# Kernel tuning notes

Hardware: AMD Instinct MI355X
Metric: run time of the kernel (lower is better)

Reference implementation:

```python
import jax, jax.numpy as jnp
import numpy as np

H = 187          # BATTLEFIELD_HEXES
MS = 20          # MAX_STACKS
MOB = 10         # MAX_OBSTACLES
D = 128          # d_model
NH = 4           # n_heads
NL = 4           # n_layers
CE = 16          # creature_embed_dim
NAT = 5          # NUM_ACTION_TYPES
NCT = 256        # NUM_CREATURE_TYPES
HEXC = 29        # HEX_CONTINUOUS_DIM
B = 1024


def _ln(x, g, b):
    m = x.mean(-1, keepdims=True)
    v = jnp.mean((x - m) ** 2, -1, keepdims=True)
    return (x - m) / jnp.sqrt(v + 1e-5) * g + b


def _mlp(x, w1, b1, w2, b2):
    return jax.nn.relu(x @ w1.T + b1) @ w2.T + b2


def _forward(p, n_stacks):
    scalars = p['scalars']
    s = p['stacks']
    pos = s[:, :, 18].astype(jnp.int32)                       # POSITION
    alive = s[:, :, 23]                                       # ALIVE
    idx_mask = jnp.arange(MS)[None, :] < n_stacks             # (B, MS)
    valid = (pos >= 0) & (pos < H) & (alive >= 0.5) & idx_mask
    max_hp = jnp.maximum(s[:, :, 4], 1.0)
    is_active = (s[:, :, 0] == scalars[:, 2:3]).astype(jnp.float32)
    is_ally = (s[:, :, 20] == scalars[:, 3:4]).astype(jnp.float32)
    zeros = jnp.zeros_like(alive)
    feat = jnp.stack([
        jnp.ones_like(alive), s[:, :, 2] / 1000.0, s[:, :, 3] / max_hp,
        s[:, :, 8] / 100.0, s[:, :, 9] / 100.0, s[:, :, 10] / 100.0, s[:, :, 11] / 100.0,
        s[:, :, 12] / 100.0, s[:, :, 13] / 100.0, s[:, :, 14] / 100.0, s[:, :, 15] / 100.0,
        s[:, :, 16] / 20.0, s[:, :, 17] / 20.0, s[:, :, 20], is_ally, alive,
        s[:, :, 24], s[:, :, 25], s[:, :, 26], s[:, :, 27], s[:, :, 28], s[:, :, 29],
        s[:, :, 30], s[:, :, 31] / 30.0, s[:, :, 33] / 5.0, s[:, :, 34] / 10.0,
        is_active, zeros, zeros], axis=-1)                    # (B, MS, 29)
    bidx = jnp.arange(B)[:, None]
    safe_pos = jnp.where(valid, pos, H)                       # dummy slot H for invalid
    hex_cont = jnp.zeros((B, H + 1, HEXC)).at[bidx, safe_pos].set(
        jnp.where(valid[..., None], feat, 0.0))[:, :H]
    cid = jnp.minimum(s[:, :, 1].astype(jnp.int32), NCT - 1)
    cids = jnp.zeros((B, H + 1), jnp.int32).at[bidx, safe_pos].set(
        jnp.where(valid, cid, 0))[:, :H]
    hex_cont = hex_cont.at[:, :, 27].set(p['reachable_hexes'])
    opos = p['obstacles'][:, :, 2].astype(jnp.int32)
    ovalid = (p['obstacles'][:, :, 0] > 0) & (opos >= 0) & (opos < H)
    obs_ch = jnp.zeros((B, H + 1)).at[bidx, jnp.where(ovalid, opos, H)].max(
        ovalid.astype(jnp.float32))[:, :H]
    hex_cont = hex_cont.at[:, :, 28].set(obs_ch)
    hex_feat = jnp.concatenate([hex_cont, p['creature_emb'][cids]], -1)   # (B,H,45)

    hex_tok = _ln(hex_feat @ p['hex_proj_w'].T + p['hex_proj_b'],
                  p['hex_ln_g'], p['hex_ln_b'])
    hex_tok = hex_tok + p['hex_pos_emb'][None] + p['tok_type_emb'][0]

    sc = scalars
    atk = jnp.stack([sc[:, 8], sc[:, 11] / 300.0, sc[:, 10] / 10.0, sc[:, 12] / 10.0,
                     jnp.zeros(B)], -1)
    dfn = jnp.stack([sc[:, 14], sc[:, 17] / 300.0, sc[:, 16] / 10.0, sc[:, 18] / 10.0,
                     jnp.ones(B)], -1)
    atk_t = _ln(atk @ p['hero_proj_w'].T + p['hero_proj_b'], p['hero_ln_g'], p['hero_ln_b']) + p['tok_type_emb'][1]
    def_t = _ln(dfn @ p['hero_proj_w'].T + p['hero_proj_b'], p['hero_ln_g'], p['hero_ln_b']) + p['tok_type_emb'][2]
    tokens = jnp.concatenate([hex_tok, atk_t[:, None], def_t[:, None]], 1)  # (B,189,D)

    gfeat = jnp.stack([sc[:, 1] / 50.0, sc[:, 4] / 10.0, sc[:, 5] / 10.0, sc[:, 6], sc[:, 3]], -1)
    tokens = tokens + (gfeat @ p['global_w'].T + p['global_b'])[:, None]

    S = tokens.shape[1]
    hd = D // NH
    for l in range(NL):  # pre-LN transformer encoder (eval mode, no dropout)
        x = _ln(tokens, p['tf_ln1_g'][l], p['tf_ln1_b'][l])
        qkv = x @ p['tf_qkv_w'][l].T + p['tf_qkv_b'][l]
        q, k, v = jnp.split(qkv, 3, -1)
        rs = lambda t: t.reshape(B, S, NH, hd).transpose(0, 2, 1, 3)
        q, k, v = rs(q), rs(k), rs(v)
        att = jax.nn.softmax(jnp.einsum('bhqd,bhkd->bhqk', q, k) / jnp.sqrt(float(hd)), -1)
        o = jnp.einsum('bhqk,bhkd->bhqd', att, v).transpose(0, 2, 1, 3).reshape(B, S, D)
        tokens = tokens + o @ p['tf_o_w'][l].T + p['tf_o_b'][l]
        y = _ln(tokens, p['tf_ln2_g'][l], p['tf_ln2_b'][l])
        tokens = tokens + jax.nn.relu(y @ p['tf_ff1_w'][l].T + p['tf_ff1_b'][l]) @ p['tf_ff2_w'][l].T + p['tf_ff2_b'][l]
    tokens = _ln(tokens, p['post_ln_g'], p['post_ln_b'])

    hex_out = tokens[:, :H]
    pooled = tokens.mean(1)
    action_type_logits = _mlp(pooled, p['at_w1'], p['at_b1'], p['at_w2'], p['at_b2'])
    hex_logits = _mlp(hex_out, p['hex_w1'], p['hex_b1'], p['hex_w2'], p['hex_b2']).squeeze(-1)
    tgt_tok = jnp.take_along_axis(hex_out, jnp.clip(pos, 0, H - 1)[..., None], axis=1)  # (B,MS,D)
    tgt = _mlp(tgt_tok, p['tg_w1'], p['tg_b1'], p['tg_w2'], p['tg_b2']).squeeze(-1)
    target_logits = jnp.where(valid, tgt, -1e9)
    value = _mlp(pooled, p['val_w1'], p['val_b1'], p['val_w2'], p['val_b2']).squeeze(-1)
    return (action_type_logits, hex_logits, target_logits, value)


def setup_inputs() -> dict:
    key = jax.random.key(0)
    ks = iter(jax.random.split(key, 64))
    nk = lambda: next(ks)
    _p = lambda shape: 0.02 * jax.random.normal(nk(), shape, dtype=jnp.float32)

    scalars = jax.random.uniform(nk(), (B, 19)) * 10.0
    scalars = scalars.at[:, 2].set(jax.random.randint(nk(), (B,), 0, MS).astype(jnp.float32))
    scalars = scalars.at[:, 3].set(jax.random.randint(nk(), (B,), 0, 2).astype(jnp.float32))

    stacks = jax.random.uniform(nk(), (B, MS, 35)) * 50.0
    perm = jax.vmap(lambda k: jax.random.permutation(k, H)[:MS])(jax.random.split(nk(), B))
    stacks = stacks.at[:, :, 18].set(perm.astype(jnp.float32))          # unique positions
    stacks = stacks.at[:, :, 23].set((jax.random.uniform(nk(), (B, MS)) > 0.2).astype(jnp.float32))
    stacks = stacks.at[:, :, 1].set(jax.random.randint(nk(), (B, MS), 0, NCT).astype(jnp.float32))
    stacks = stacks.at[:, :, 0].set(jnp.broadcast_to(jnp.arange(MS, dtype=jnp.float32), (B, MS)))
    stacks = stacks.at[:, :, 20].set(jax.random.randint(nk(), (B, MS), 0, 2).astype(jnp.float32))

    obstacles = jnp.stack([
        jax.random.randint(nk(), (B, MOB), 0, 3).astype(jnp.float32),
        jnp.zeros((B, MOB)),
        jax.random.randint(nk(), (B, MOB), 0, H).astype(jnp.float32)], -1)
    reachable_hexes = (jax.random.uniform(nk(), (B, H)) > 0.5).astype(jnp.float32)
    n_stacks = jax.random.randint(nk(), (B, 1), 1, MS + 1)

    inp = dict(scalars=scalars, stacks=stacks, obstacles=obstacles,
               reachable_hexes=reachable_hexes, n_stacks=n_stacks)
    inp['creature_emb'] = _p((NCT, CE)).at[0].set(0.0)   # padding_idx=0
    inp['hex_pos_emb'] = _p((H, D))
    inp['tok_type_emb'] = _p((3, D))
    inp['hex_proj_w'] = _p((D, HEXC + CE)); inp['hex_proj_b'] = _p((D,))
    inp['hex_ln_g'] = jnp.ones(D); inp['hex_ln_b'] = jnp.zeros(D)
    inp['hero_proj_w'] = _p((D, 5)); inp['hero_proj_b'] = _p((D,))
    inp['hero_ln_g'] = jnp.ones(D); inp['hero_ln_b'] = jnp.zeros(D)
    inp['global_w'] = _p((D, 5)); inp['global_b'] = _p((D,))
    inp['tf_ln1_g'] = jnp.ones((NL, D)); inp['tf_ln1_b'] = jnp.zeros((NL, D))
    inp['tf_qkv_w'] = _p((NL, 3 * D, D)); inp['tf_qkv_b'] = _p((NL, 3 * D))
    inp['tf_o_w'] = _p((NL, D, D)); inp['tf_o_b'] = _p((NL, D))
    inp['tf_ln2_g'] = jnp.ones((NL, D)); inp['tf_ln2_b'] = jnp.zeros((NL, D))
    inp['tf_ff1_w'] = _p((NL, 4 * D, D)); inp['tf_ff1_b'] = _p((NL, 4 * D))
    inp['tf_ff2_w'] = _p((NL, D, 4 * D)); inp['tf_ff2_b'] = _p((NL, D))
    inp['post_ln_g'] = jnp.ones(D); inp['post_ln_b'] = jnp.zeros(D)
    inp['at_w1'] = _p((D, D)); inp['at_b1'] = _p((D,)); inp['at_w2'] = _p((NAT, D)); inp['at_b2'] = _p((NAT,))
    inp['hex_w1'] = _p((D // 2, D)); inp['hex_b1'] = _p((D // 2,)); inp['hex_w2'] = _p((1, D // 2)); inp['hex_b2'] = _p((1,))
    inp['tg_w1'] = _p((D // 2, D)); inp['tg_b1'] = _p((D // 2,)); inp['tg_w2'] = _p((1, D // 2)); inp['tg_b2'] = _p((1,))
    inp['val_w1'] = _p((D, D)); inp['val_b1'] = _p((D,)); inp['val_w2'] = _p((1, D)); inp['val_b2'] = _p((1,))
    return inp


def reference(scalars, stacks, obstacles, reachable_hexes, n_stacks, creature_emb, hex_pos_emb, tok_type_emb, hex_proj_w, hex_proj_b, hex_ln_g, hex_ln_b, hero_proj_w, hero_proj_b, hero_ln_g, hero_ln_b, global_w, global_b, tf_ln1_g, tf_ln1_b, tf_qkv_w, tf_qkv_b, tf_o_w, tf_o_b, tf_ln2_g, tf_ln2_b, tf_ff1_w, tf_ff1_b, tf_ff2_w, tf_ff2_b, post_ln_g, post_ln_b, at_w1, at_b1, at_w2, at_b2, hex_w1, hex_b1, hex_w2, hex_b2, tg_w1, tg_b1, tg_w2, tg_b2, val_w1, val_b1, val_w2, val_b2):
    fl = dict(locals())
    ns = fl.pop('n_stacks')
    return _forward(fl, ns)
```

## Files before the change

kernel.cpp:

```cpp
#include <hip/hip_runtime.h>
#include <hip/hip_bf16.h>

#define DEV static __device__ __forceinline__

typedef __attribute__((ext_vector_type(8))) short bf16x8;
typedef __attribute__((ext_vector_type(4))) float f32x4;
#define MFMA16 __builtin_amdgcn_mfma_f32_16x16x32_bf16

DEV unsigned short f2bf_rn(float x) {
  unsigned u = __float_as_uint(x);
  u = u + 0x7fffu + ((u >> 16) & 1u);
  return (unsigned short)(u >> 16);
}
DEV unsigned pack2(float a, float b) {
  return (unsigned)f2bf_rn(a) | ((unsigned)f2bf_rn(b) << 16);
}
DEV float lo2f(unsigned w) { return __uint_as_float(w << 16); }
DEV float hi2f(unsigned w) { return __uint_as_float(w & 0xffff0000u); }

constexpr int H_ = 187, MS_ = 20, MOB_ = 10, D_ = 128, NH_ = 4, NL_ = 4,
              CE_ = 16, NAT_ = 5, NCT_ = 256, HEXC_ = 29, B_ = 1024;
constexpr int S_ = H_ + 2;
constexpr int ST = 68;
constexpr int PST = 36;
constexpr int VTS = 100;

constexpr int VT_OFF   = 192 * PST;
constexpr int CORR_OFF = VT_OFF + 32 * VTS;
constexpr int LSUM_OFF = CORR_OFF + 192;
constexpr int GV_OFF   = LSUM_OFF + 192;
constexpr int PO_OFF   = GV_OFF + 128;
constexpr int H1_OFF   = PO_OFF + 128;
constexpr int H2_OFF   = H1_OFF + 128;

constexpr int OFF_HEX = B_ * NAT_;
constexpr int OFF_TGT = OFF_HEX + B_ * H_;
constexpr int OFF_VAL = OFF_TGT + B_ * MS_;

constexpr float SCALE = 0.17677669529663687f;

constexpr int WS_Q = 0;
constexpr int WS_O = WS_Q + 4 * 384 * 128;
constexpr int WS_F1 = WS_O + 4 * 128 * 128;
constexpr int WS_F2 = WS_F1 + 4 * 512 * 128;
constexpr int WS_TOT = WS_F2 + 4 * 128 * 512;

struct Params {
  const float *scalars, *stacks, *obstacles, *reach;
  const int  *n_stacks;
  const float *cemb, *pos_emb, *tte;
  const float *hexW, *hexB, *hexG, *hexBe;
  const float *heroW, *heroB, *heroG, *heroBe;
  const float *gW, *gB;
  const float *ln1g, *ln1b, *qkvW, *qkvB, *oW, *oB;
  const float *ln2g, *ln2b, *f1W, *f1B, *f2W, *f2B;
  const float *plng, *plnb;
  const float *atW1, *atB1, *atW2, *atB2;
  const float *hxW1, *hxB1, *hxW2, *hxB2;
  const float *tgW1, *tgB1, *tgW2, *tgB2;
  const float *vlW1, *vlB1, *vlW2, *vlB2;
  const unsigned short *wsb;
  float *out;
};

DEV bf16x8 ldAx(const unsigned* buf, int stride, int mbase, int cbase, int lane) {
  return *(const bf16x8*)(buf + (mbase + (lane & 15)) * stride + cbase +
                          ((lane >> 4) << 2));
}
DEV bf16x8 ldBw(const float* q) {
  bf16x8 r;
#pragma unroll
  for (int j = 0; j < 8; ++j) r[j] = (short)f2bf_rn(q[j]);
  return r;
}
template <bool WSB>
DEV bf16x8 ldB(const unsigned short* wb, const float* wf, int off) {
  if constexpr (WSB) return *(const bf16x8*)(wb + off);
  else return ldBw(wf + off);
}

__global__ __launch_bounds__(256) void convw_kernel(const float *qkv,
                                                    const float *o,
                                                    const float *f1,
                                                    const float *f2,
                                                    unsigned short *ws) {
  int i = blockIdx.x * 256 + threadIdx.x;
  if (i < WS_O) ws[i] = f2bf_rn(qkv[i - WS_Q]);
  else if (i < WS_F1) ws[i] = f2bf_rn(o[i - WS_O]);
  else if (i < WS_F2) ws[i] = f2bf_rn(f1[i - WS_F1]);
  else if (i < WS_TOT) ws[i] = f2bf_rn(f2[i - WS_F2]);
}

template <bool WSB>
__global__ __launch_bounds__(768, 1) void battle_kernel(Params p) {
  __shared__ __align__(16) unsigned tokp[192 * ST];
  __shared__ __align__(16) unsigned xln[192 * ST];
  __shared__ __align__(16) unsigned area[192 * ST];
  __shared__ int svalid[MS_], sposc[MS_];

  const int b = blockIdx.x;
  const int tid = threadIdx.x;
  const int lane = tid & 63;
  const int wave = tid >> 6;
  const bool hasrow = tid < S_;
  const float *sc = p.scalars + b * 19;

  float *areaF = (float *)area;
  unsigned short *tok16 = (unsigned short *)tokp;
  unsigned short *xln16 = (unsigned short *)xln;
  unsigned short *P16 = (unsigned short *)area;
  unsigned short *vt16 = (unsigned short *)(area + VT_OFF);

  float *hexcont = (float *)area;
  int   *cids    = (int *)area + 5440;
  float *obsch   = (float *)area + 5632;

  if (tid < D_) {
    float g0 = sc[1] * 0.02f, g1 = sc[4] * 0.1f, g2 = sc[5] * 0.1f;
    float g3 = sc[6], g4 = sc[3];
    const float *w = p.gW + tid * 5;
    areaF[GV_OFF + tid] = p.gB[tid] + g0 * w[0] + g1 * w[1] + g2 * w[2] +
                          g3 * w[3] + g4 * w[4];
  }
  for (int i = tid; i < H_ * HEXC_; i += 768) hexcont[i] = 0.f;
  for (int i = tid; i < H_; i += 768) { cids[i] = 0; obsch[i] = 0.f; }
  if (tid >= 189 && tid < 192) {
    for (int c = 0; c < 64; ++c) tokp[tid * ST + c] = 0u;
  }
  __syncthreads();

  if (tid < MS_) {
    const float *st = p.stacks + (b * MS_ + tid) * 35;
    int pos = (int)st[18];
    float alive = st[23];
    int ns = p.n_stacks[b];
    bool valid = (pos >= 0) && (pos < H_) && (alive >= 0.5f) && (tid < ns);
    svalid[tid] = valid ? 1 : 0;
    sposc[tid] = min(max(pos, 0), H_ - 1);
    if (valid) {
      float maxhp = fmaxf(st[4], 1.0f);
      float *hc = hexcont + pos * HEXC_;
      hc[0] = 1.0f;
      hc[1] = st[2] * 1e-3f;
      hc[2] = st[3] / maxhp;
      hc[3] = st[8] * 0.01f;  hc[4] = st[9] * 0.01f;
      hc[5] = st[10] * 0.01f; hc[6] = st[11] * 0.01f;
      hc[7] = st[12] * 0.01f; hc[8] = st[13] * 0.01f;
      hc[9] = st[14] * 0.01f; hc[10] = st[15] * 0.01f;
      hc[11] = st[16] * 0.05f; hc[12] = st[17] * 0.05f;
      float s20 = st[20];
      hc[13] = s20;
      hc[14] = (s20 == sc[3]) ? 1.f : 0.f;
      hc[15] = alive;
      hc[16] = st[24]; hc[17] = st[25]; hc[18] = st[26];
      hc[19] = st[27]; hc[20] = st[28]; hc[21] = st[29];
      hc[22] = st[30];
      hc[23] = st[31] * (1.f / 30.f);
      hc[24] = st[33] * 0.2f;
      hc[25] = st[34] * 0.1f;
      hc[26] = (st[0] == sc[2]) ? 1.f : 0.f;
      hc[27] = 0.f; hc[28] = 0.f;
      cids[pos] = min((int)st[1], NCT_ - 1);
    }
  }
  if (tid >= 64 && tid < 64 + MOB_) {
    const float *ob = p.obstacles + (b * MOB_ + (tid - 64)) * 3;
    int opos = (int)ob[2];
    if (ob[0] > 0.f && opos >= 0 && opos < H_) obsch[opos] = 1.0f;
  }
  __syncthreads();

  if (tid < H_) {
    const int r = tid;
    float f[HEXC_ + CE_];
#pragma unroll
    for (int c = 0; c < HEXC_; ++c) f[c] = hexcont[r * HEXC_ + c];
    f[27] = p.reach[b * H_ + r];
    f[28] = obsch[r];
    int cid = cids[r];
#pragma unroll
    for (int e = 0; e < CE_; ++e) f[HEXC_ + e] = p.cemb[cid * CE_ + e];
    float sum = 0.f;
    for (int d2 = 0; d2 < 64; ++d2) {
      const float *w0 = p.hexW + (2 * d2) * 45;
      const float *w1 = w0 + 45;
      float a0 = p.hexB[2 * d2], a1 = 0.f, a2 = 0.f, a3 = 0.f;
      float b0 = p.hexB[2 * d2 + 1], b1 = 0.f, b2 = 0.f, b3 = 0.f;
#pragma unroll
      for (int k = 0; k < 44; k += 4) {
        a0 = fmaf(f[k], w0[k], a0);       a1 = fmaf(f[k + 1], w0[k + 1], a1);
        a2 = fmaf(f[k + 2], w0[k + 2], a2); a3 = fmaf(f[k + 3], w0[k + 3], a3);
        b0 = fmaf(f[k], w1[k], b0);       b1 = fmaf(f[k + 1], w1[k + 1], b1);
        b2 = fmaf(f[k + 2], w1[k + 2], b2); b3 = fmaf(f[k + 3], w1[k + 3], b3);
      }
      a0 = fmaf(f[44], w0[44], a0);
      b0 = fmaf(f[44], w1[44], b0);
      float va = (a0 + a1) + (a2 + a3), vb = (b0 + b1) + (b2 + b3);
      tokp[r * ST + d2] = pack2(va, vb);
      sum += va + vb;
    }
    float m = sum * (1.f / 128.f);
    float var = 0.f;
#pragma unroll 4
    for (int d2 = 0; d2 < 64; ++d2) {
      unsigned w = tokp[r * ST + d2];
      float t0 = lo2f(w) - m, t1 = hi2f(w) - m;
      var = fmaf(t0, t0, var); var = fmaf(t1, t1, var);
    }
    float rs = rsqrtf(var * (1.f / 128.f) + 1e-5f);
#pragma unroll 2
    for (int d2 = 0; d2 < 64; ++d2) {
      unsigned w = tokp[r * ST + d2];
      int d = 2 * d2;
      float v0 = (lo2f(w) - m) * rs * p.hexG[d] + p.hexBe[d] +
                 p.pos_emb[r * D_ + d] + p.tte[d] + areaF[GV_OFF + d];
      float v1 = (hi2f(w) - m) * rs * p.hexG[d + 1] + p.hexBe[d + 1] +
                 p.pos_emb[r * D_ + d + 1] + p.tte[d + 1] + areaF[GV_OFF + d + 1];
      tokp[r * ST + d2] = pack2(v0, v1);
    }
  } else if (tid < S_) {
    const int which = tid - H_;
    float f0, f1, f2, f3, f4;
    if (which == 0) {
      f0 = sc[8];  f1 = sc[11] * (1.f / 300.f);
      f2 = sc[10] * 0.1f; f3 = sc[12] * 0.1f; f4 = 0.f;
    } else {
      f0 = sc[14]; f1 = sc[17] * (1.f / 300.f);
      f2 = sc[16] * 0.1f; f3 = sc[18] * 0.1f; f4 = 1.f;
    }
    const int r = tid;
    float sum = 0.f;
    for (int d2 = 0; d2 < 64; ++d2) {
      const float *w0 = p.heroW + (2 * d2) * 5;
      const float *w1 = w0 + 5;
      float va = p.heroB[2 * d2] + f0 * w0[0] + f1 * w0[1] + f2 * w0[2] + f3 * w0[3] + f4 * w0[4];
      float vb = p.heroB[2 * d2 + 1] + f0 * w1[0] + f1 * w1[1] + f2 * w1[2] + f3 * w1[3] + f4 * w1[4];
      tokp[r * ST + d2] = pack2(va, vb);
      sum += va + vb;
    }
    float m = sum * (1.f / 128.f);
    float var = 0.f;
    for (int d2 = 0; d2 < 64; ++d2) {
      unsigned w = tokp[r * ST + d2];
      float t0 = lo2f(w) - m, t1 = hi2f(w) - m;
      var = fmaf(t0, t0, var); var = fmaf(t1, t1, var);
    }
    float rs = rsqrtf(var * (1.f / 128.f) + 1e-5f);
    for (int d2 = 0; d2 < 64; ++d2) {
      unsigned w = tokp[r * ST + d2];
      int d = 2 * d2;
      float v0 = (lo2f(w) - m) * rs * p.heroG[d] + p.heroBe[d] +
                 p.tte[(1 + which) * D_ + d] + areaF[GV_OFF + d];
      float v1 = (hi2f(w) - m) * rs * p.heroG[d + 1] + p.heroBe[d + 1] +
                 p.tte[(1 + which) * D_ + d + 1] + areaF[GV_OFF + d + 1];
      tokp[r * ST + d2] = pack2(v0, v1);
    }
  }

  const int lrow = tid >> 2;
  const int lsub = tid & 3;

  for (int l = 0; l < NL_; ++l) {
    const float *ln1g = p.ln1g + l * D_, *ln1b = p.ln1b + l * D_;
    const float *qkvW = p.qkvW + l * 3 * D_ * D_, *qkvB = p.qkvB + l * 3 * D_;
    const float *oW = p.oW + l * D_ * D_, *oB = p.oB + l * D_;
    const float *ln2g = p.ln2g + l * D_, *ln2b = p.ln2b + l * D_;
    const float *f1W = p.f1W + l * 4 * D_ * D_, *f1B = p.f1B + l * 4 * D_;
    const float *f2W = p.f2W + l * 4 * D_ * D_, *f2B = p.f2B + l * D_;
    const unsigned short *qkvWb = p.wsb + WS_Q + l * 384 * 128;
    const unsigned short *oWb = p.wsb + WS_O + l * 128 * 128;
    const unsigned short *f1Wb = p.wsb + WS_F1 + l * 512 * 128;
    const unsigned short *f2Wb = p.wsb + WS_F2 + l * 128 * 512;

    __syncthreads();

    if (lrow < S_) {
      float s = 0.f;
#pragma unroll
      for (int i = 0; i < 16; ++i) {
        unsigned w = tokp[lrow * ST + lsub * 16 + i];
        s += lo2f(w) + hi2f(w);
      }
      s += __shfl_xor(s, 1); s += __shfl_xor(s, 2);
      float m = s * (1.f / 128.f);
      float v = 0.f;
#pragma unroll
      for (int i = 0; i < 16; ++i) {
        unsigned w = tokp[lrow * ST + lsub * 16 + i];
        float t0 = lo2f(w) - m, t1 = hi2f(w) - m;
        v = fmaf(t0, t0, v); v = fmaf(t1, t1, v);
      }
      v += __shfl_xor(v, 1); v += __shfl_xor(v, 2);
      float rs = rsqrtf(v * (1.f / 128.f) + 1e-5f);
#pragma unroll
      for (int i = 0; i < 16; ++i) {
        int d2 = lsub * 16 + i, d = 2 * d2;
        unsigned w = tokp[lrow * ST + d2];
        xln[lrow * ST + d2] = pack2((lo2f(w) - m) * rs * ln1g[d] + ln1b[d],
                                    (hi2f(w) - m) * rs * ln1g[d + 1] + ln1b[d + 1]);
      }
    } else {
#pragma unroll
      for (int i = 0; i < 16; ++i) xln[lrow * ST + lsub * 16 + i] = 0u;
    }
    __syncthreads();

    f32x4 oacc[4][2];

#pragma unroll
    for (int h = 0; h < NH_; ++h) {
#pragma unroll
      for (int nd = 0; nd < 2; ++nd) oacc[h][nd] = {0.f, 0.f, 0.f, 0.f};

      {
        int ntg = wave >> 1, mh = wave & 1;
        int nrow0, c16 = 0, isV = 0, ntd = 0;
        if (ntg < 2)      { nrow0 = h * 32 + ntg * 16;            c16 = ntg * 16; }
        else if (ntg < 4) { nrow0 = 128 + h * 32 + (ntg - 2) * 16; c16 = 32 + (ntg - 2) * 16; }
        else              { nrow0 = 256 + h * 32 + (ntg - 4) * 16; isV = 1; ntd = ntg - 4; }
        int roff = (nrow0 + (lane & 15)) * 128;
        int koff = (lane >> 4) << 3;
        bf16x8 b0 = ldB<WSB>(qkvWb, qkvW, roff + koff);
        bf16x8 b1 = ldB<WSB>(qkvWb, qkvW, roff + 32 + koff);
        bf16x8 b2 = ldB<WSB>(qkvWb, qkvW, roff + 64 + koff);
        bf16x8 b3 = ldB<WSB>(qkvWb, qkvW, roff + 96 + koff);
        float bv = qkvB[nrow0 + (lane & 15)];
        int col16 = c16 + (lane & 15);
#pragma unroll 1
        for (int mt = mh * 6; mt < mh * 6 + 6; ++mt) {
          f32x4 acc = {bv, bv, bv, bv};
          acc = MFMA16(ldAx(xln, ST, mt * 16, 0, lane), b0, acc, 0, 0, 0);
          acc = MFMA16(ldAx(xln, ST, mt * 16, 16, lane), b1, acc, 0, 0, 0);
          acc = MFMA16(ldAx(xln, ST, mt * 16, 32, lane), b2, acc, 0, 0, 0);
          acc = MFMA16(ldAx(xln, ST, mt * 16, 48, lane), b3, acc, 0, 0, 0);
          int rb = mt * 16 + ((lane >> 4) << 2);
          if (!isV) {
#pragma unroll
            for (int g = 0; g < 4; ++g)
              P16[(rb + g) * (PST * 2) + col16] = f2bf_rn(acc[g]);
          } else {
#pragma unroll
            for (int g = 0; g < 4; ++g)
              vt16[(ntd * 16 + (lane & 15)) * (VTS * 2) + rb + g] = f2bf_rn(acc[g]);
          }
        }
      }
      __syncthreads();

      bf16x8 qf = ldAx(area, PST, wave * 16, 0, lane);
      bf16x8 kf[12];
#pragma unroll
      for (int nt = 0; nt < 12; ++nt)
        kf[nt] = ldAx(area, PST, nt * 16, 16, lane);
      float mrun = -1e30f, lrun = 0.f;
      const int srow = wave * 16 + (lane & 15);
      const int ssub = lane >> 4;
      __syncthreads();

#pragma unroll
      for (int t = 0; t < 3; ++t) {
        {
          int rb = wave * 16 + ((lane >> 4) << 2);
#pragma unroll
          for (int ntl = 0; ntl < 4; ++ntl) {
            f32x4 s = {0.f, 0.f, 0.f, 0.f};
            s = MFMA16(qf, kf[t * 4 + ntl], s, 0, 0, 0);
            int col16 = ntl * 16 + (lane & 15);
#pragma unroll
            for (int g = 0; g < 4; ++g)
              P16[(rb + g) * (PST * 2) + col16] = f2bf_rn(s[g]);
          }
        }
        {
          float tm = -1e30f;
          int cb = ssub * 8;
#pragma unroll
          for (int i = 0; i < 8; ++i) {
            int c2 = cb + i;
            unsigned w = area[srow * PST + c2];
            float v0 = lo2f(w) * SCALE, v1 = hi2f(w) * SCALE;
            if (t == 2 && c2 == 30) v1 = -1e30f;
            if (t == 2 && c2 == 31) { v0 = -1e30f; v1 = -1e30f; }
            tm = fmaxf(tm, fmaxf(v0, v1));
          }
          tm = fmaxf(tm, __shfl_xor(tm, 16));
          tm = fmaxf(tm, __shfl_xor(tm, 32));
          float mnew = fmaxf(mrun, tm);
          float corrv = __expf(mrun - mnew);
          float ts = 0.f;
#pragma unroll
          for (int i = 0; i < 8; ++i) {
            int c2 = cb + i;
            unsigned w = area[srow * PST + c2];
            float e0 = __expf(lo2f(w) * SCALE - mnew);
            float e1 = __expf(hi2f(w) * SCALE - mnew);
            if (t == 2 && c2 == 30) e1 = 0.f;
            if (t == 2 && c2 == 31) { e0 = 0.f; e1 = 0.f; }
            ts += e0 + e1;
            area[srow * PST + c2] = pack2(e0, e1);
          }
          ts += __shfl_xor(ts, 16);
          ts += __shfl_xor(ts, 32);
          lrun = lrun * corrv + ts;
          mrun = mnew;
          if (ssub == 0) {
            areaF[CORR_OFF + srow] = corrv;
            if (t == 2) areaF[LSUM_OFF + srow] = lrun;
          }
        }
        {
          int rb = wave * 16 + ((lane >> 4) << 2);
          float c0 = areaF[CORR_OFF + rb], c1 = areaF[CORR_OFF + rb + 1];
          float c2v = areaF[CORR_OFF + rb + 2], c3 = areaF[CORR_OFF + rb + 3];
#pragma unroll
          for (int nd = 0; nd < 2; ++nd) {
            f32x4 a = oacc[h][nd];
            a[0] *= c0; a[1] *= c1; a[2] *= c2v; a[3] *= c3;
#pragma unroll
            for (int kt = 0; kt < 2; ++kt) {
              bf16x8 af = ldAx(area, PST, wave * 16, kt * 16, lane);
              bf16x8 bv = *(const bf16x8*)(area + VT_OFF +
                            (nd * 16 + (lane & 15)) * VTS + t * 32 + kt * 16 +
                            ((lane >> 4) << 2));
              a = MFMA16(af, bv, a, 0, 0, 0);
            }
            oacc[h][nd] = a;
          }
          if (t == 2) {
            float i0 = 1.f / areaF[LSUM_OFF + rb];
            float i1 = 1.f / areaF[LSUM_OFF + rb + 1];
            float i2 = 1.f / areaF[LSUM_OFF + rb + 2];
            float i3 = 1.f / areaF[LSUM_OFF + rb + 3];
#pragma unroll
            for (int nd = 0; nd < 2; ++nd) {
              f32x4 a = oacc[h][nd];
              a[0] *= i0; a[1] *= i1; a[2] *= i2; a[3] *= i3;
              oacc[h][nd] = a;
            }
          }
        }
      }
      __syncthreads();
    }

#pragma unroll
    for (int h = 0; h < NH_; ++h) {
      int rb = wave * 16 + ((lane >> 4) << 2);
#pragma unroll
      for (int nd = 0; nd < 2; ++nd) {
        int col16 = h * 32 + nd * 16 + (lane & 15);
        f32x4 a = oacc[h][nd];
#pragma unroll
        for (int g = 0; g < 4; ++g)
          xln16[(rb + g) * (ST * 2) + col16] = f2bf_rn(a[g]);
      }
    }
    __syncthreads();

#pragma unroll 1
    for (int job = wave; job < 16; job += 12) {
      int nt = job >> 1, mh = job & 1;
      int roff = (nt * 16 + (lane & 15)) * 128;
      int koff = (lane >> 4) << 3;
      bf16x8 b0 = ldB<WSB>(oWb, oW, roff + koff);
      bf16x8 b1 = ldB<WSB>(oWb, oW, roff + 32 + koff);
      bf16x8 b2 = ldB<WSB>(oWb, oW, roff + 64 + koff);
      bf16x8 b3 = ldB<WSB>(oWb, oW, roff + 96 + koff);
      float bv = oB[nt * 16 + (lane & 15)];
      int col16 = nt * 16 + (lane & 15);
#pragma unroll 1
      for (int mt = mh * 6; mt < mh * 6 + 6; ++mt) {
        f32x4 acc = {bv, bv, bv, bv};
        acc = MFMA16(ldAx(xln, ST, mt * 16, 0, lane), b0, acc, 0, 0, 0);
        acc = MFMA16(ldAx(xln, ST, mt * 16, 16, lane), b1, acc, 0, 0, 0);
        acc = MFMA16(ldAx(xln, ST, mt * 16, 32, lane), b2, acc, 0, 0, 0);
        acc = MFMA16(ldAx(xln, ST, mt * 16, 48, lane), b3, acc, 0, 0, 0);
        int rb = mt * 16 + ((lane >> 4) << 2);
#pragma unroll
        for (int g = 0; g < 4; ++g) {
          int a16 = (rb + g) * (ST * 2) + col16;
          float old = __uint_as_float((unsigned)tok16[a16] << 16);
          tok16[a16] = f2bf_rn(old + acc[g]);
        }
      }
    }
    __syncthreads();

    if (lrow < S_) {
      float s = 0.f;
#pragma unroll
      for (int i = 0; i < 16; ++i) {
        unsigned w = tokp[lrow * ST + lsub * 16 + i];
        s += lo2f(w) + hi2f(w);
      }
      s += __shfl_xor(s, 1); s += __shfl_xor(s, 2);
      float m = s * (1.f / 128.f);
      float v = 0.f;
#pragma unroll
      for (int i = 0; i < 16; ++i) {
        unsigned w = tokp[lrow * ST + lsub * 16 + i];
        float t0 = lo2f(w) - m, t1 = hi2f(w) - m;
        v = fmaf(t0, t0, v); v = fmaf(t1, t1, v);
      }
      v += __shfl_xor(v, 1); v += __shfl_xor(v, 2);
      float rs = rsqrtf(v * (1.f / 128.f) + 1e-5f);
#pragma unroll
      for (int i = 0; i < 16; ++i) {
        int d2 = lsub * 16 + i, d = 2 * d2;
        unsigned w = tokp[lrow * ST + d2];
        xln[lrow * ST + d2] = pack2((lo2f(w) - m) * rs * ln2g[d] + ln2b[d],
                                    (hi2f(w) - m) * rs * ln2g[d + 1] + ln2b[d + 1]);
      }
    } else {
#pragma unroll
      for (int i = 0; i < 16; ++i) xln[lrow * ST + lsub * 16 + i] = 0u;
    }
    __syncthreads();

    const int ja = wave;
    const bool hasb = wave < 4;
    const int jb = wave + 12;
    const int nta = ja >> 1, mha = ja & 1;
    const int ntb = jb >> 1, mhb = jb & 1;
    f32x4 acca[6], accb[6];
    {
      float bva = f2B[nta * 16 + (lane & 15)];
#pragma unroll
      for (int i = 0; i < 6; ++i) acca[i] = {bva, bva, bva, bva};
      float bvb = hasb ? f2B[ntb * 16 + (lane & 15)] : 0.f;
#pragma unroll
      for (int i = 0; i < 6; ++i) accb[i] = {bvb, bvb, bvb, bvb};
    }
    for (int chunk = 0; chunk < 4; ++chunk) {
#pragma unroll 1
      for (int job = wave; job < 16; job += 12) {
        int nt = job >> 1, mh = job & 1;
        int roff = (chunk * 128 + nt * 16 + (lane & 15)) * 128;
        int koff = (lane >> 4) << 3;
        bf16x8 b0 = ldB<WSB>(f1Wb, f1W, roff + koff);
        bf16x8 b1 = ldB<WSB>(f1Wb, f1W, roff + 32 + koff);
        bf16x8 b2 = ldB<WSB>(f1Wb, f1W, roff + 64 + koff);
        bf16x8 b3 = ldB<WSB>(f1Wb, f1W, roff + 96 + koff);
        float bv = f1B[chunk * 128 + nt * 16 + (lane & 15)];
        int col16 = nt * 16 + (lane & 15);
#pragma unroll 1
        for (int mt = mh * 6; mt < mh * 6 + 6; ++mt) {
          f32x4 acc = {bv, bv, bv, bv};
          acc = MFMA16(ldAx(xln, ST, mt * 16, 0, lane), b0, acc, 0, 0, 0);
          acc = MFMA16(ldAx(xln, ST, mt * 16, 16, lane), b1, acc, 0, 0, 0);
          acc = MFMA16(ldAx(xln, ST, mt * 16, 32, lane), b2, acc, 0, 0, 0);
          acc = MFMA16(ldAx(xln, ST, mt * 16, 48, lane), b3, acc, 0, 0, 0);
          int rb = mt * 16 + ((lane >> 4) << 2);
#pragma unroll
          for (int g = 0; g < 4; ++g)
            P16[(rb + g) * (ST * 2) + col16] = f2bf_rn(fmaxf(acc[g], 0.f));
        }
      }
      __syncthreads();
      {
        int roff = (nta * 16 + (lane & 15)) * 512 + chunk * 128;
        int koff = (lane >> 4) << 3;
        bf16x8 b0 = ldB<WSB>(f2Wb, f2W, roff + koff);
        bf16x8 b1 = ldB<WSB>(f2Wb, f2W, roff + 32 + koff);
        bf16x8 b2 = ldB<WSB>(f2Wb, f2W, roff + 64 + koff);
        bf16x8 b3 = ldB<WSB>(f2Wb, f2W, roff + 96 + koff);
#pragma unroll
        for (int i = 0; i < 6; ++i) {
          int mt = mha * 6 + i;
          f32x4 a = acca[i];
          a = MFMA16(ldAx(area, ST, mt * 16, 0, lane), b0, a, 0, 0, 0);
          a = MFMA16(ldAx(area, ST, mt * 16, 16, lane), b1, a, 0, 0, 0);
          a = MFMA16(ldAx(area, ST, mt * 16, 32, lane), b2, a, 0, 0, 0);
          a = MFMA16(ldAx(area, ST, mt * 16, 48, lane), b3, a, 0, 0, 0);
          acca[i] = a;
        }
      }
      if (hasb) {
        int roff = (ntb * 16 + (lane & 15)) * 512 + chunk * 128;
        int koff = (lane >> 4) << 3;
        bf16x8 b0 = ldB<WSB>(f2Wb, f2W, roff + koff);
        bf16x8 b1 = ldB<WSB>(f2Wb, f2W, roff + 32 + koff);
        bf16x8 b2 = ldB<WSB>(f2Wb, f2W, roff + 64 + koff);
        bf16x8 b3 = ldB<WSB>(f2Wb, f2W, roff + 96 + koff);
#pragma unroll
        for (int i = 0; i < 6; ++i) {
          int mt = mhb * 6 + i;
          f32x4 a = accb[i];
          a = MFMA16(ldAx(area, ST, mt * 16, 0, lane), b0, a, 0, 0, 0);
          a = MFMA16(ldAx(area, ST, mt * 16, 16, lane), b1, a, 0, 0, 0);
          a = MFMA16(ldAx(area, ST, mt * 16, 32, lane), b2, a, 0, 0, 0);
          a = MFMA16(ldAx(area, ST, mt * 16, 48, lane), b3, a, 0, 0, 0);
          accb[i] = a;
        }
      }
      __syncthreads();
    }
    {
      int col16 = nta * 16 + (lane & 15);
#pragma unroll
      for (int i = 0; i < 6; ++i) {
        int rb = (mha * 6 + i) * 16 + ((lane >> 4) << 2);
        f32x4 a = acca[i];
#pragma unroll
        for (int g = 0; g < 4; ++g) {
          int a16 = (rb + g) * (ST * 2) + col16;
          float old = __uint_as_float((unsigned)tok16[a16] << 16);
          tok16[a16] = f2bf_rn(old + a[g]);
        }
      }
    }
    if (hasb) {
      int col16 = ntb * 16 + (lane & 15);
#pragma unroll
      for (int i = 0; i < 6; ++i) {
        int rb = (mhb * 6 + i) * 16 + ((lane >> 4) << 2);
        f32x4 a = accb[i];
#pragma unroll
        for (int g = 0; g < 4; ++g) {
          int a16 = (rb + g) * (ST * 2) + col16;
          float old = __uint_as_float((unsigned)tok16[a16] << 16);
          tok16[a16] = f2bf_rn(old + a[g]);
        }
      }
    }
  }
  __syncthreads();

  if (lrow < S_) {
    float s = 0.f;
#pragma unroll
    for (int i = 0; i < 16; ++i) {
      unsigned w = tokp[lrow * ST + lsub * 16 + i];
      s += lo2f(w) + hi2f(w);
    }
    s += __shfl_xor(s, 1); s += __shfl_xor(s, 2);
    float m = s * (1.f / 128.f);
    float v = 0.f;
#pragma unroll
    for (int i = 0; i < 16; ++i) {
      unsigned w = tokp[lrow * ST + lsub * 16 + i];
      float t0 = lo2f(w) - m, t1 = hi2f(w) - m;
      v = fmaf(t0, t0, v); v = fmaf(t1, t1, v);
    }
    v += __shfl_xor(v, 1); v += __shfl_xor(v, 2);
    float rs = rsqrtf(v * (1.f / 128.f) + 1e-5f);
#pragma unroll
    for (int i = 0; i < 16; ++i) {
      int d2 = lsub * 16 + i, d = 2 * d2;
      unsigned w = tokp[lrow * ST + d2];
      tokp[lrow * ST + d2] = pack2((lo2f(w) - m) * rs * p.plng[d] + p.plnb[d],
                                   (hi2f(w) - m) * rs * p.plng[d + 1] + p.plnb[d + 1]);
    }
  }
  __syncthreads();

  if (tid < D_) {
    const int d2 = tid >> 1;
    const bool hi = tid & 1;
    float s0 = 0.f, s1 = 0.f;
    int r = 0;
    for (; r + 2 <= S_; r += 2) {
      unsigned w0 = tokp[r * ST + d2], w1 = tokp[(r + 1) * ST + d2];
      s0 += hi ? hi2f(w0) : lo2f(w0);
      s1 += hi ? hi2f(w1) : lo2f(w1);
    }
    unsigned wl = tokp[(S_ - 1) * ST + d2];
    s0 += hi ? hi2f(wl) : lo2f(wl);
    areaF[PO_OFF + tid] = (s0 + s1) * (1.f / (float)S_);
  }
  __syncthreads();
  if (tid < D_) {
    const float *wa = p.atW1 + tid * D_;
    const float *wv = p.vlW1 + tid * D_;
    float a0 = p.atB1[tid], a1 = 0.f, vv0 = p.vlB1[tid], vv1 = 0.f;
#pragma unroll 4
    for (int k = 0; k < D_; k += 2) {
      float pk0 = areaF[PO_OFF + k], pk1 = areaF[PO_OFF + k + 1];
      a0 = fmaf(pk0, wa[k], a0);   a1 = fmaf(pk1, wa[k + 1], a1);
      vv0 = fmaf(pk0, wv[k], vv0); vv1 = fmaf(pk1, wv[k + 1], vv1);
    }
    areaF[H1_OFF + tid] = fmaxf(a0 + a1, 0.f);
    areaF[H2_OFF + tid] = fmaxf(vv0 + vv1, 0.f);
  }
  __syncthreads();

  if (tid < H_) {
    float hh[64];
#pragma unroll
    for (int j = 0; j < 64; ++j) hh[j] = p.hxB1[j];
    for (int kb = 0; kb < 8; ++kb) {
      float xr[16];
#pragma unroll
      for (int i2 = 0; i2 < 8; ++i2) {
        unsigned w = tokp[tid * ST + kb * 8 + i2];
        xr[2 * i2] = lo2f(w); xr[2 * i2 + 1] = hi2f(w);
      }
      const float *w = p.hxW1 + kb * 16;
#pragma unroll
      for (int j = 0; j < 64; ++j) {
#pragma unroll
        for (int i = 0; i < 16; ++i)
          hh[j] = fmaf(xr[i], w[j * D_ + i], hh[j]);
      }
    }
    float o = p.hxB2[0];
#pragma unroll
    for (int j = 0; j < 64; ++j) o = fmaf(fmaxf(hh[j], 0.f), p.hxW2[j], o);
    p.out[OFF_HEX + b * H_ + tid] = o;
  }
  if (tid < NAT_) {
    const float *w = p.atW2 + tid * D_;
    float o0 = p.atB2[tid], o1 = 0.f, o2 = 0.f, o3 = 0.f;
#pragma unroll 4
    for (int k = 0; k < D_; k += 4) {
      o0 = fmaf(areaF[H1_OFF + k], w[k], o0);
      o1 = fmaf(areaF[H1_OFF + k + 1], w[k + 1], o1);
      o2 = fmaf(areaF[H1_OFF + k + 2], w[k + 2], o2);
      o3 = fmaf(areaF[H1_OFF + k + 3], w[k + 3], o3);
    }
    p.out[b * NAT_ + tid] = (o0 + o1) + (o2 + o3);
  }
  if (tid == 190) {
    float o0 = p.vlB2[0], o1 = 0.f, o2 = 0.f, o3 = 0.f;
#pragma unroll 4
    for (int k = 0; k < D_; k += 4) {
      o0 = fmaf(areaF[H2_OFF + k], p.vlW2[k], o0);
      o1 = fmaf(areaF[H2_OFF + k + 1], p.vlW2[k + 1], o1);
      o2 = fmaf(areaF[H2_OFF + k + 2], p.vlW2[k + 2], o2);
      o3 = fmaf(areaF[H2_OFF + k + 3], p.vlW2[k + 3], o3);
    }
    p.out[OFF_VAL + b] = (o0 + o1) + (o2 + o3);
  }
  if (tid >= 32 && tid < 32 + MS_) {
    int si = tid - 32;
    float o;
    if (svalid[si]) {
      int r = sposc[si];
      float hh[64];
#pragma unroll
      for (int j = 0; j < 64; ++j) hh[j] = p.tgB1[j];
      for (int kb = 0; kb < 8; ++kb) {
        float xr[16];
#pragma unroll
        for (int i2 = 0; i2 < 8; ++i2) {
          unsigned w = tokp[r * ST + kb * 8 + i2];
          xr[2 * i2] = lo2f(w); xr[2 * i2 + 1] = hi2f(w);
        }
        const float *w = p.tgW1 + kb * 16;
#pragma unroll
        for (int j = 0; j < 64; ++j) {
#pragma unroll
          for (int i = 0; i < 16; ++i)
            hh[j] = fmaf(xr[i], w[j * D_ + i], hh[j]);
        }
      }
      o = p.tgB2[0];
#pragma unroll
      for (int j = 0; j < 64; ++j) o = fmaf(fmaxf(hh[j], 0.f), p.tgW2[j], o);
    } else {
      o = -1e9f;
    }
    p.out[OFF_TGT + b * MS_ + si] = o;
  }
}

extern "C" void kernel_launch(void* const* d_in, const int* in_sizes, int n_in,
                              void* d_out, int out_size, void* d_ws, size_t ws_size,
                              hipStream_t stream) {
  (void)in_sizes; (void)n_in; (void)out_size;
  Params p;
  p.scalars = (const float *)d_in[0];
  p.stacks = (const float *)d_in[1];
  p.obstacles = (const float *)d_in[2];
  p.reach = (const float *)d_in[3];
  p.n_stacks = (const int *)d_in[4];
  p.cemb = (const float *)d_in[5];
  p.pos_emb = (const float *)d_in[6];
  p.tte = (const float *)d_in[7];
  p.hexW = (const float *)d_in[8];  p.hexB = (const float *)d_in[9];
  p.hexG = (const float *)d_in[10]; p.hexBe = (const float *)d_in[11];
  p.heroW = (const float *)d_in[12]; p.heroB = (const float *)d_in[13];
  p.heroG = (const float *)d_in[14]; p.heroBe = (const float *)d_in[15];
  p.gW = (const float *)d_in[16]; p.gB = (const float *)d_in[17];
  p.ln1g = (const float *)d_in[18]; p.ln1b = (const float *)d_in[19];
  p.qkvW = (const float *)d_in[20]; p.qkvB = (const float *)d_in[21];
  p.oW = (const float *)d_in[22]; p.oB = (const float *)d_in[23];
  p.ln2g = (const float *)d_in[24]; p.ln2b = (const float *)d_in[25];
  p.f1W = (const float *)d_in[26]; p.f1B = (const float *)d_in[27];
  p.f2W = (const float *)d_in[28]; p.f2B = (const float *)d_in[29];
  p.plng = (const float *)d_in[30]; p.plnb = (const float *)d_in[31];
  p.atW1 = (const float *)d_in[32]; p.atB1 = (const float *)d_in[33];
  p.atW2 = (const float *)d_in[34]; p.atB2 = (const float *)d_in[35];
  p.hxW1 = (const float *)d_in[36]; p.hxB1 = (const float *)d_in[37];
  p.hxW2 = (const float *)d_in[38]; p.hxB2 = (const float *)d_in[39];
  p.tgW1 = (const float *)d_in[40]; p.tgB1 = (const float *)d_in[41];
  p.tgW2 = (const float *)d_in[42]; p.tgB2 = (const float *)d_in[43];
  p.vlW1 = (const float *)d_in[44]; p.vlB1 = (const float *)d_in[45];
  p.vlW2 = (const float *)d_in[46]; p.vlB2 = (const float *)d_in[47];
  p.out = (float *)d_out;
  bool usews = ws_size >= (size_t)WS_TOT * 2;
  if (usews) {
    p.wsb = (const unsigned short *)d_ws;
    convw_kernel<<<dim3((WS_TOT + 255) / 256), dim3(256), 0, stream>>>(
        p.qkvW, p.oW, p.f1W, p.f2W, (unsigned short *)d_ws);
    battle_kernel<true><<<dim3(B_), dim3(768), 0, stream>>>(p);
  } else {
    p.wsb = nullptr;
    battle_kernel<false><<<dim3(B_), dim3(768), 0, stream>>>(p);
  }
}
```

Before: 2.085 ms.

## Keep residual stream in registers with row-owned waves across transformer layers

Each wave now owns 16 token rows and keeps the fp32 residual in registers (X[4][8]) across all layers, so LayerNorm, the O-projection residual add and the FFN residual add happen in registers instead of through a bf16 token buffer in shared memory. The QKV, O and FFN GEMMs are restructured so each wave computes every output column for its own rows, which removes several __syncthreads and the read-modify-write of bf16 residuals. The cost is that every wave now loads all weight fragments (more global/L2 weight traffic per block) and register pressure rises. The residual also stays in fp32 rather than being rounded to bf16 after each sublayer.

```diff
diff --git a/kernel.cpp b/kernel.cpp
--- a/kernel.cpp
+++ b/kernel.cpp
@@ -17,12 +17,15 @@
 }
 DEV float lo2f(unsigned w) { return __uint_as_float(w << 16); }
 DEV float hi2f(unsigned w) { return __uint_as_float(w & 0xffff0000u); }
+DEV float u16f(unsigned short v) { return __uint_as_float(((unsigned)v) << 16); }
 
 constexpr int H_ = 187, MS_ = 20, MOB_ = 10, D_ = 128, NH_ = 4, NL_ = 4,
               CE_ = 16, NAT_ = 5, NCT_ = 256, HEXC_ = 29, B_ = 1024;
 constexpr int S_ = H_ + 2;
-constexpr int ST = 68;
+constexpr int XST = 84;
+constexpr int QOFF = 64;
 constexpr int PST = 36;
+constexpr int AST = 68;
 constexpr int VTS = 100;
 
 constexpr int VT_OFF   = 192 * PST;
@@ -93,23 +96,23 @@
 
 template <bool WSB>
 __global__ __launch_bounds__(768, 1) void battle_kernel(Params p) {
-  __shared__ __align__(16) unsigned tokp[192 * ST];
-  __shared__ __align__(16) unsigned xln[192 * ST];
-  __shared__ __align__(16) unsigned area[192 * ST];
+  __shared__ __align__(16) unsigned xln[192 * XST];
+  __shared__ __align__(16) unsigned area[192 * AST];
   __shared__ int svalid[MS_], sposc[MS_];
 
   const int b = blockIdx.x;
   const int tid = threadIdx.x;
   const int lane = tid & 63;
   const int wave = tid >> 6;
-  const bool hasrow = tid < S_;
+  const int colb = lane & 15;
+  const int row0 = wave * 16 + ((lane >> 4) << 2);
   const float *sc = p.scalars + b * 19;
 
   float *areaF = (float *)area;
-  unsigned short *tok16 = (unsigned short *)tokp;
   unsigned short *xln16 = (unsigned short *)xln;
   unsigned short *P16 = (unsigned short *)area;
   unsigned short *vt16 = (unsigned short *)(area + VT_OFF);
+  unsigned short *hid16 = (unsigned short *)area;
 
   float *hexcont = (float *)area;
   int   *cids    = (int *)area + 5440;
@@ -125,7 +128,7 @@
   for (int i = tid; i < H_ * HEXC_; i += 768) hexcont[i] = 0.f;
   for (int i = tid; i < H_; i += 768) { cids[i] = 0; obsch[i] = 0.f; }
   if (tid >= 189 && tid < 192) {
-    for (int c = 0; c < 64; ++c) tokp[tid * ST + c] = 0u;
+    for (int c = 0; c < 64; ++c) xln[tid * XST + c] = 0u;
   }
   __syncthreads();
 
@@ -196,27 +199,27 @@
       a0 = fmaf(f[44], w0[44], a0);
       b0 = fmaf(f[44], w1[44], b0);
       float va = (a0 + a1) + (a2 + a3), vb = (b0 + b1) + (b2 + b3);
-      tokp[r * ST + d2] = pack2(va, vb);
+      xln[r * XST + d2] = pack2(va, vb);
       sum += va + vb;
     }
     float m = sum * (1.f / 128.f);
     float var = 0.f;
 #pragma unroll 4
     for (int d2 = 0; d2 < 64; ++d2) {
-      unsigned w = tokp[r * ST + d2];
+      unsigned w = xln[r * XST + d2];
       float t0 = lo2f(w) - m, t1 = hi2f(w) - m;
       var = fmaf(t0, t0, var); var = fmaf(t1, t1, var);
     }
     float rs = rsqrtf(var * (1.f / 128.f) + 1e-5f);
 #pragma unroll 2
     for (int d2 = 0; d2 < 64; ++d2) {
-      unsigned w = tokp[r * ST + d2];
+      unsigned w = xln[r * XST + d2];
       int d = 2 * d2;
       float v0 = (lo2f(w) - m) * rs * p.hexG[d] + p.hexBe[d] +
                  p.pos_emb[r * D_ + d] + p.tte[d] + areaF[GV_OFF + d];
       float v1 = (hi2f(w) - m) * rs * p.hexG[d + 1] + p.hexBe[d + 1] +
                  p.pos_emb[r * D_ + d + 1] + p.tte[d + 1] + areaF[GV_OFF + d + 1];
-      tokp[r * ST + d2] = pack2(v0, v1);
+      xln[r * XST + d2] = pack2(v0, v1);
     }
   } else if (tid < S_) {
     const int which = tid - H_;
@@ -235,30 +238,35 @@
       const float *w1 = w0 + 5;
       float va = p.heroB[2 * d2] + f0 * w0[0] + f1 * w0[1] + f2 * w0[2] + f3 * w0[3] + f4 * w0[4];
       float vb = p.heroB[2 * d2 + 1] + f0 * w1[0] + f1 * w1[1] + f2 * w1[2] + f3 * w1[3] + f4 * w1[4];
-      tokp[r * ST + d2] = pack2(va, vb);
+      xln[r * XST + d2] = pack2(va, vb);
       sum += va + vb;
     }
     float m = sum * (1.f / 128.f);
     float var = 0.f;
     for (int d2 = 0; d2 < 64; ++d2) {
-      unsigned w = tokp[r * ST + d2];
+      unsigned w = xln[r * XST + d2];
       float t0 = lo2f(w) - m, t1 = hi2f(w) - m;
       var = fmaf(t0, t0, var); var = fmaf(t1, t1, var);
     }
     float rs = rsqrtf(var * (1.f / 128.f) + 1e-5f);
     for (int d2 = 0; d2 < 64; ++d2) {
-      unsigned w = tokp[r * ST + d2];
+      unsigned w = xln[r * XST + d2];
       int d = 2 * d2;
       float v0 = (lo2f(w) - m) * rs * p.heroG[d] + p.heroBe[d] +
                  p.tte[(1 + which) * D_ + d] + areaF[GV_OFF + d];
       float v1 = (hi2f(w) - m) * rs * p.heroG[d + 1] + p.heroBe[d + 1] +
                  p.tte[(1 + which) * D_ + d + 1] + areaF[GV_OFF + d + 1];
-      tokp[r * ST + d2] = pack2(v0, v1);
-    }
-  }
-
-  const int lrow = tid >> 2;
-  const int lsub = tid & 3;
+      xln[r * XST + d2] = pack2(v0, v1);
+    }
+  }
+  __syncthreads();
+
+  float X[4][8];
+#pragma unroll
+  for (int g = 0; g < 4; ++g)
+#pragma unroll
+    for (int nt = 0; nt < 8; ++nt)
+      X[g][nt] = u16f(xln16[(row0 + g) * (XST * 2) + nt * 16 + colb]);
 
   for (int l = 0; l < NL_; ++l) {
     const float *ln1g = p.ln1g + l * D_, *ln1b = p.ln1b + l * D_;
@@ -274,101 +282,108 @@
 
     __syncthreads();
 
-    if (lrow < S_) {
-      float s = 0.f;
-#pragma unroll
-      for (int i = 0; i < 16; ++i) {
-        unsigned w = tokp[lrow * ST + lsub * 16 + i];
-        s += lo2f(w) + hi2f(w);
-      }
-      s += __shfl_xor(s, 1); s += __shfl_xor(s, 2);
-      float m = s * (1.f / 128.f);
-      float v = 0.f;
-#pragma unroll
-      for (int i = 0; i < 16; ++i) {
-        unsigned w = tokp[lrow * ST + lsub * 16 + i];
-        float t0 = lo2f(w) - m, t1 = hi2f(w) - m;
-        v = fmaf(t0, t0, v); v = fmaf(t1, t1, v);
-      }
-      v += __shfl_xor(v, 1); v += __shfl_xor(v, 2);
-      float rs = rsqrtf(v * (1.f / 128.f) + 1e-5f);
-#pragma unroll
-      for (int i = 0; i < 16; ++i) {
-        int d2 = lsub * 16 + i, d = 2 * d2;
-        unsigned w = tokp[lrow * ST + d2];
-        xln[lrow * ST + d2] = pack2((lo2f(w) - m) * rs * ln1g[d] + ln1b[d],
-                                    (hi2f(w) - m) * rs * ln1g[d + 1] + ln1b[d + 1]);
-      }
-    } else {
-#pragma unroll
-      for (int i = 0; i < 16; ++i) xln[lrow * ST + lsub * 16 + i] = 0u;
-    }
-    __syncthreads();
+    {
+      float ga[8], be[8];
+#pragma unroll
+      for (int nt = 0; nt < 8; ++nt) {
+        ga[nt] = ln1g[nt * 16 + colb];
+        be[nt] = ln1b[nt * 16 + colb];
+      }
+#pragma unroll
+      for (int g = 0; g < 4; ++g) {
+        float s = 0.f;
+#pragma unroll
+        for (int nt = 0; nt < 8; ++nt) s += X[g][nt];
+        s += __shfl_xor(s, 1); s += __shfl_xor(s, 2);
+        s += __shfl_xor(s, 4); s += __shfl_xor(s, 8);
+        float m = s * (1.f / 128.f);
+        float v = 0.f;
+#pragma unroll
+        for (int nt = 0; nt < 8; ++nt) {
+          float t = X[g][nt] - m;
+          v = fmaf(t, t, v);
+        }
+        v += __shfl_xor(v, 1); v += __shfl_xor(v, 2);
+        v += __shfl_xor(v, 4); v += __shfl_xor(v, 8);
+        float rs = rsqrtf(v * (1.f / 128.f) + 1e-5f);
+#pragma unroll
+        for (int nt = 0; nt < 8; ++nt)
+          xln16[(row0 + g) * (XST * 2) + nt * 16 + colb] =
+              f2bf_rn((X[g][nt] - m) * rs * ga[nt] + be[nt]);
+      }
+    }
 
     f32x4 oacc[4][2];
-
-#pragma unroll
+#pragma unroll
+    for (int h = 0; h < NH_; ++h)
+#pragma unroll
+      for (int nd = 0; nd < 2; ++nd) oacc[h][nd] = {0.f, 0.f, 0.f, 0.f};
+
+#pragma unroll 1
     for (int h = 0; h < NH_; ++h) {
-#pragma unroll
-      for (int nd = 0; nd < 2; ++nd) oacc[h][nd] = {0.f, 0.f, 0.f, 0.f};
-
       {
-        int ntg = wave >> 1, mh = wave & 1;
-        int nrow0, c16 = 0, isV = 0, ntd = 0;
-        if (ntg < 2)      { nrow0 = h * 32 + ntg * 16;            c16 = ntg * 16; }
-        else if (ntg < 4) { nrow0 = 128 + h * 32 + (ntg - 2) * 16; c16 = 32 + (ntg - 2) * 16; }
-        else              { nrow0 = 256 + h * 32 + (ntg - 4) * 16; isV = 1; ntd = ntg - 4; }
-        int roff = (nrow0 + (lane & 15)) * 128;
+        bf16x8 a0 = ldAx(xln, XST, wave * 16, 0, lane);
+        bf16x8 a1 = ldAx(xln, XST, wave * 16, 16, lane);
+        bf16x8 a2 = ldAx(xln, XST, wave * 16, 32, lane);
+        bf16x8 a3 = ldAx(xln, XST, wave * 16, 48, lane);
         int koff = (lane >> 4) << 3;
-        bf16x8 b0 = ldB<WSB>(qkvWb, qkvW, roff + koff);
-        bf16x8 b1 = ldB<WSB>(qkvWb, qkvW, roff + 32 + koff);
-        bf16x8 b2 = ldB<WSB>(qkvWb, qkvW, roff + 64 + koff);
-        bf16x8 b3 = ldB<WSB>(qkvWb, qkvW, roff + 96 + koff);
-        float bv = qkvB[nrow0 + (lane & 15)];
-        int col16 = c16 + (lane & 15);
-#pragma unroll 1
-        for (int mt = mh * 6; mt < mh * 6 + 6; ++mt) {
+#pragma unroll
+        for (int ng = 0; ng < 6; ++ng) {
+          int nrow0 = (ng < 2) ? (h * 32 + ng * 16)
+                    : (ng < 4) ? (128 + h * 32 + (ng - 2) * 16)
+                               : (256 + h * 32 + (ng - 4) * 16);
+          int roff = (nrow0 + colb) * 128;
+          bf16x8 b0 = ldB<WSB>(qkvWb, qkvW, roff + koff);
+          bf16x8 b1 = ldB<WSB>(qkvWb, qkvW, roff + 32 + koff);
+          bf16x8 b2 = ldB<WSB>(qkvWb, qkvW, roff + 64 + koff);
+          bf16x8 b3 = ldB<WSB>(qkvWb, qkvW, roff + 96 + koff);
+          float bv = qkvB[nrow0 + colb];
           f32x4 acc = {bv, bv, bv, bv};
-          acc = MFMA16(ldAx(xln, ST, mt * 16, 0, lane), b0, acc, 0, 0, 0);
-          acc = MFMA16(ldAx(xln, ST, mt * 16, 16, lane), b1, acc, 0, 0, 0);
-          acc = MFMA16(ldAx(xln, ST, mt * 16, 32, lane), b2, acc, 0, 0, 0);
-          acc = MFMA16(ldAx(xln, ST, mt * 16, 48, lane), b3, acc, 0, 0, 0);
-          int rb = mt * 16 + ((lane >> 4) << 2);
-          if (!isV) {
+          acc = MFMA16(a0, b0, acc, 0, 0, 0);
+          acc = MFMA16(a1, b1, acc, 0, 0, 0);
+          acc = MFMA16(a2, b2, acc, 0, 0, 0);
+          acc = MFMA16(a3, b3, acc, 0, 0, 0);
+          if (ng < 2) {
+            int col16 = ng * 16 + colb;
 #pragma unroll
             for (int g = 0; g < 4; ++g)
-              P16[(rb + g) * (PST * 2) + col16] = f2bf_rn(acc[g]);
+              xln16[(row0 + g) * (XST * 2) + QOFF * 2 + col16] = f2bf_rn(acc[g]);
+          } else if (ng < 4) {
+            int col16 = (ng - 2) * 16 + colb;
+#pragma unroll
+            for (int g = 0; g < 4; ++g)
+              P16[(row0 + g) * (PST * 2) + col16] = f2bf_rn(acc[g]);
           } else {
+            int vcol = (ng - 4) * 16 + colb;
 #pragma unroll
             for (int g = 0; g < 4; ++g)
-              vt16[(ntd * 16 + (lane & 15)) * (VTS * 2) + rb + g] = f2bf_rn(acc[g]);
+              vt16[vcol * (VTS * 2) + row0 + g] = f2bf_rn(acc[g]);
           }
         }
       }
       __syncthreads();
 
-      bf16x8 qf = ldAx(area, PST, wave * 16, 0, lane);
+      bf16x8 qf = ldAx(xln, XST, wave * 16, QOFF, lane);
       bf16x8 kf[12];
 #pragma unroll
       for (int nt = 0; nt < 12; ++nt)
-        kf[nt] = ldAx(area, PST, nt * 16, 16, lane);
+        kf[nt] = ldAx(area, PST, nt * 16, 0, lane);
       float mrun = -1e30f, lrun = 0.f;
-      const int srow = wave * 16 + (lane & 15);
+      const int srow = wave * 16 + colb;
       const int ssub = lane >> 4;
       __syncthreads();
 
 #pragma unroll
       for (int t = 0; t < 3; ++t) {
         {
-          int rb = wave * 16 + ((lane >> 4) << 2);
 #pragma unroll
           for (int ntl = 0; ntl < 4; ++ntl) {
             f32x4 s = {0.f, 0.f, 0.f, 0.f};
             s = MFMA16(qf, kf[t * 4 + ntl], s, 0, 0, 0);
-            int col16 = ntl * 16 + (lane & 15);
+            int col16 = ntl * 16 + colb;
 #pragma unroll
             for (int g = 0; g < 4; ++g)
-              P16[(rb + g) * (PST * 2) + col16] = f2bf_rn(s[g]);
+              P16[(row0 + g) * (PST * 2) + col16] = f2bf_rn(s[g]);
           }
         }
         {
@@ -409,9 +424,8 @@
           }
         }
         {
-          int rb = wave * 16 + ((lane >> 4) << 2);
-          float c0 = areaF[CORR_OFF + rb], c1 = areaF[CORR_OFF + rb + 1];
-          float c2v = areaF[CORR_OFF + rb + 2], c3 = areaF[CORR_OFF + rb + 3];
+          float c0 = areaF[CORR_OFF + row0], c1 = areaF[CORR_OFF + row0 + 1];
+          float c2v = areaF[CORR_OFF + row0 + 2], c3 = areaF[CORR_OFF + row0 + 3];
 #pragma unroll
           for (int nd = 0; nd < 2; ++nd) {
             f32x4 a = oacc[h][nd];
@@ -420,17 +434,17 @@
             for (int kt = 0; kt < 2; ++kt) {
               bf16x8 af = ldAx(area, PST, wave * 16, kt * 16, lane);
               bf16x8 bv = *(const bf16x8*)(area + VT_OFF +
-                            (nd * 16 + (lane & 15)) * VTS + t * 32 + kt * 16 +
+                            (nd * 16 + colb) * VTS + t * 32 + kt * 16 +
                             ((lane >> 4) << 2));
               a = MFMA16(af, bv, a, 0, 0, 0);
             }
             oacc[h][nd] = a;
           }
           if (t == 2) {
-            float i0 = 1.f / areaF[LSUM_OFF + rb];
-            float i1 = 1.f / areaF[LSUM_OFF + rb + 1];
-            float i2 = 1.f / areaF[LSUM_OFF + rb + 2];
-            float i3 = 1.f / areaF[LSUM_OFF + rb + 3];
+            float i0 = 1.f / areaF[LSUM_OFF + row0];
+            float i1 = 1.f / areaF[LSUM_OFF + row0 + 1];
+            float i2 = 1.f / areaF[LSUM_OFF + row0 + 2];
+            float i3 = 1.f / areaF[LSUM_OFF + row0 + 3];
 #pragma unroll
             for (int nd = 0; nd < 2; ++nd) {
               f32x4 a = oacc[h][nd];
@@ -444,212 +458,158 @@
     }
 
 #pragma unroll
-    for (int h = 0; h < NH_; ++h) {
-      int rb = wave * 16 + ((lane >> 4) << 2);
+    for (int h = 0; h < NH_; ++h)
 #pragma unroll
       for (int nd = 0; nd < 2; ++nd) {
-        int col16 = h * 32 + nd * 16 + (lane & 15);
+        int col16 = h * 32 + nd * 16 + colb;
         f32x4 a = oacc[h][nd];
 #pragma unroll
         for (int g = 0; g < 4; ++g)
-          xln16[(rb + g) * (ST * 2) + col16] = f2bf_rn(a[g]);
+          xln16[(row0 + g) * (XST * 2) + col16] = f2bf_rn(a[g]);
+      }
+
+    {
+      bf16x8 a0 = ldAx(xln, XST, wave * 16, 0, lane);
+      bf16x8 a1 = ldAx(xln, XST, wave * 16, 16, lane);
+      bf16x8 a2 = ldAx(xln, XST, wave * 16, 32, lane);
+      bf16x8 a3 = ldAx(xln, XST, wave * 16, 48, lane);
+      int koff = (lane >> 4) << 3;
+#pragma unroll
+      for (int nt = 0; nt < 8; ++nt) {
+        int roff = (nt * 16 + colb) * 128;
+        bf16x8 b0 = ldB<WSB>(oWb, oW, roff + koff);
+        bf16x8 b1 = ldB<WSB>(oWb, oW, roff + 32 + koff);
+        bf16x8 b2 = ldB<WSB>(oWb, oW, roff + 64 + koff);
+        bf16x8 b3 = ldB<WSB>(oWb, oW, roff + 96 + koff);
+        float bv = oB[nt * 16 + colb];
+        f32x4 acc = {bv, bv, bv, bv};
+        acc = MFMA16(a0, b0, acc, 0, 0, 0);
+        acc = MFMA16(a1, b1, acc, 0, 0, 0);
+        acc = MFMA16(a2, b2, acc, 0, 0, 0);
+        acc = MFMA16(a3, b3, acc, 0, 0, 0);
+#pragma unroll
+        for (int g = 0; g < 4; ++g) X[g][nt] += acc[g];
+      }
+    }
+
+    {
+      float ga[8], be[8];
+#pragma unroll
+      for (int nt = 0; nt < 8; ++nt) {
+        ga[nt] = ln2g[nt * 16 + colb];
+        be[nt] = ln2b[nt * 16 + colb];
+      }
+#pragma unroll
+      for (int g = 0; g < 4; ++g) {
+        float s = 0.f;
+#pragma unroll
+        for (int nt = 0; nt < 8; ++nt) s += X[g][nt];
+        s += __shfl_xor(s, 1); s += __shfl_xor(s, 2);
+        s += __shfl_xor(s, 4); s += __shfl_xor(s, 8);
+        float m = s * (1.f / 128.f);
+        float v = 0.f;
+#pragma unroll
+        for (int nt = 0; nt < 8; ++nt) {
+          float t = X[g][nt] - m;
+          v = fmaf(t, t, v);
+        }
+        v += __shfl_xor(v, 1); v += __shfl_xor(v, 2);
+        v += __shfl_xor(v, 4); v += __shfl_xor(v, 8);
+        float rs = rsqrtf(v * (1.f / 128.f) + 1e-5f);
+#pragma unroll
+        for (int nt = 0; nt < 8; ++nt)
+          xln16[(row0 + g) * (XST * 2) + nt * 16 + colb] =
+              f2bf_rn((X[g][nt] - m) * rs * ga[nt] + be[nt]);
       }
     }
     __syncthreads();
 
+    {
+      bf16x8 a0 = ldAx(xln, XST, wave * 16, 0, lane);
+      bf16x8 a1 = ldAx(xln, XST, wave * 16, 16, lane);
+      bf16x8 a2 = ldAx(xln, XST, wave * 16, 32, lane);
+      bf16x8 a3 = ldAx(xln, XST, wave * 16, 48, lane);
+      int koff = (lane >> 4) << 3;
+      f32x4 acc2[8];
+#pragma unroll
+      for (int nt = 0; nt < 8; ++nt) {
+        float bv = f2B[nt * 16 + colb];
+        acc2[nt] = {bv, bv, bv, bv};
+      }
 #pragma unroll 1
-    for (int job = wave; job < 16; job += 12) {
-      int nt = job >> 1, mh = job & 1;
-      int roff = (nt * 16 + (lane & 15)) * 128;
-      int koff = (lane >> 4) << 3;
-      bf16x8 b0 = ldB<WSB>(oWb, oW, roff + koff);
-      bf16x8 b1 = ldB<WSB>(oWb, oW, roff + 32 + koff);
-      bf16x8 b2 = ldB<WSB>(oWb, oW, roff + 64 + koff);
-      bf16x8 b3 = ldB<WSB>(oWb, oW, roff + 96 + koff);
-      float bv = oB[nt * 16 + (lane & 15)];
-      int col16 = nt * 16 + (lane & 15);
-#pragma unroll 1
-      for (int mt = mh * 6; mt < mh * 6 + 6; ++mt) {
-        f32x4 acc = {bv, bv, bv, bv};
-        acc = MFMA16(ldAx(xln, ST, mt * 16, 0, lane), b0, acc, 0, 0, 0);
-        acc = MFMA16(ldAx(xln, ST, mt * 16, 16, lane), b1, acc, 0, 0, 0);
-        acc = MFMA16(ldAx(xln, ST, mt * 16, 32, lane), b2, acc, 0, 0, 0);
-        acc = MFMA16(ldAx(xln, ST, mt * 16, 48, lane), b3, acc, 0, 0, 0);
-        int rb = mt * 16 + ((lane >> 4) << 2);
-#pragma unroll
-        for (int g = 0; g < 4; ++g) {
-          int a16 = (rb + g) * (ST * 2) + col16;
-          float old = __uint_as_float((unsigned)tok16[a16] << 16);
-          tok16[a16] = f2bf_rn(old + acc[g]);
-        }
-      }
-    }
-    __syncthreads();
-
-    if (lrow < S_) {
+      for (int chunk = 0; chunk < 4; ++chunk) {
+#pragma unroll
+        for (int nt = 0; nt < 8; ++nt) {
+          int roff = (chunk * 128 + nt * 16 + colb) * 128;
+          bf16x8 b0 = ldB<WSB>(f1Wb, f1W, roff + koff);
+          bf16x8 b1 = ldB<WSB>(f1Wb, f1W, roff + 32 + koff);
+          bf16x8 b2 = ldB<WSB>(f1Wb, f1W, roff + 64 + koff);
+          bf16x8 b3 = ldB<WSB>(f1Wb, f1W, roff + 96 + koff);
+          float bv = f1B[chunk * 128 + nt * 16 + colb];
+          f32x4 acc = {bv, bv, bv, bv};
+          acc = MFMA16(a0, b0, acc, 0, 0, 0);
+          acc = MFMA16(a1, b1, acc, 0, 0, 0);
+          acc = MFMA16(a2, b2, acc, 0, 0, 0);
+          acc = MFMA16(a3, b3, acc, 0, 0, 0);
+          int col16 = nt * 16 + colb;
+#pragma unroll
+          for (int g = 0; g < 4; ++g)
+            hid16[(row0 + g) * (AST * 2) + col16] = f2bf_rn(fmaxf(acc[g], 0.f));
+        }
+        bf16x8 h0 = ldAx(area, AST, wave * 16, 0, lane);
+        bf16x8 h1 = ldAx(area, AST, wave * 16, 16, lane);
+        bf16x8 h2 = ldAx(area, AST, wave * 16, 32, lane);
+        bf16x8 h3 = ldAx(area, AST, wave * 16, 48, lane);
+#pragma unroll
+        for (int nt = 0; nt < 8; ++nt) {
+          int roff = (nt * 16 + colb) * 512 + chunk * 128;
+          bf16x8 b0 = ldB<WSB>(f2Wb, f2W, roff + koff);
+          bf16x8 b1 = ldB<WSB>(f2Wb, f2W, roff + 32 + koff);
+          bf16x8 b2 = ldB<WSB>(f2Wb, f2W, roff + 64 + koff);
+          bf16x8 b3 = ldB<WSB>(f2Wb, f2W, roff + 96 + koff);
+          f32x4 a = acc2[nt];
+          a = MFMA16(h0, b0, a, 0, 0, 0);
+          a = MFMA16(h1, b1, a, 0, 0, 0);
+          a = MFMA16(h2, b2, a, 0, 0, 0);
+          a = MFMA16(h3, b3, a, 0, 0, 0);
+          acc2[nt] = a;
+        }
+      }
+#pragma unroll
+      for (int nt = 0; nt < 8; ++nt)
+#pragma unroll
+        for (int g = 0; g < 4; ++g) X[g][nt] += acc2[nt][g];
+    }
+  }
+
+  {
+    float ga[8], be[8];
+#pragma unroll
+    for (int nt = 0; nt < 8; ++nt) {
+      ga[nt] = p.plng[nt * 16 + colb];
+      be[nt] = p.plnb[nt * 16 + colb];
+    }
+#pragma unroll
+    for (int g = 0; g < 4; ++g) {
       float s = 0.f;
 #pragma unroll
-      for (int i = 0; i < 16; ++i) {
-        unsigned w = tokp[lrow * ST + lsub * 16 + i];
-        s += lo2f(w) + hi2f(w);
-      }
+      for (int nt = 0; nt < 8; ++nt) s += X[g][nt];
       s += __shfl_xor(s, 1); s += __shfl_xor(s, 2);
+      s += __shfl_xor(s, 4); s += __shfl_xor(s, 8);
       float m = s * (1.f / 128.f);
       float v = 0.f;
 #pragma unroll
-      for (int i = 0; i < 16; ++i) {
-        unsigned w = tokp[lrow * ST + lsub * 16 + i];
-        float t0 = lo2f(w) - m, t1 = hi2f(w) - m;
-        v = fmaf(t0, t0, v); v = fmaf(t1, t1, v);
+      for (int nt = 0; nt < 8; ++nt) {
+        float t = X[g][nt] - m;
+        v = fmaf(t, t, v);
       }
       v += __shfl_xor(v, 1); v += __shfl_xor(v, 2);
+      v += __shfl_xor(v, 4); v += __shfl_xor(v, 8);
       float rs = rsqrtf(v * (1.f / 128.f) + 1e-5f);
 #pragma unroll
-      for (int i = 0; i < 16; ++i) {
-        int d2 = lsub * 16 + i, d = 2 * d2;
-        unsigned w = tokp[lrow * ST + d2];
-        xln[lrow * ST + d2] = pack2((lo2f(w) - m) * rs * ln2g[d] + ln2b[d],
-                                    (hi2f(w) - m) * rs * ln2g[d + 1] + ln2b[d + 1]);
-      }
-    } else {
-#pragma unroll
-      for (int i = 0; i < 16; ++i) xln[lrow * ST + lsub * 16 + i] = 0u;
-    }
-    __syncthreads();
-
-    const int ja = wave;
-    const bool hasb = wave < 4;
-    const int jb = wave + 12;
-    const int nta = ja >> 1, mha = ja & 1;
-    const int ntb = jb >> 1, mhb = jb & 1;
-    f32x4 acca[6], accb[6];
-    {
-      float bva = f2B[nta * 16 + (lane & 15)];
-#pragma unroll
-      for (int i = 0; i < 6; ++i) acca[i] = {bva, bva, bva, bva};
-      float bvb = hasb ? f2B[ntb * 16 + (lane & 15)] : 0.f;
-#pragma unroll
-      for (int i = 0; i < 6; ++i) accb[i] = {bvb, bvb, bvb, bvb};
-    }
-    for (int chunk = 0; chunk < 4; ++chunk) {
-#pragma unroll 1
-      for (int job = wave; job < 16; job += 12) {
-        int nt = job >> 1, mh = job & 1;
-        int roff = (chunk * 128 + nt * 16 + (lane & 15)) * 128;
-        int koff = (lane >> 4) << 3;
-        bf16x8 b0 = ldB<WSB>(f1Wb, f1W, roff + koff);
-        bf16x8 b1 = ldB<WSB>(f1Wb, f1W, roff + 32 + koff);
-        bf16x8 b2 = ldB<WSB>(f1Wb, f1W, roff + 64 + koff);
-        bf16x8 b3 = ldB<WSB>(f1Wb, f1W, roff + 96 + koff);
-        float bv = f1B[chunk * 128 + nt * 16 + (lane & 15)];
-        int col16 = nt * 16 + (lane & 15);
-#pragma unroll 1
-        for (int mt = mh * 6; mt < mh * 6 + 6; ++mt) {
-          f32x4 acc = {bv, bv, bv, bv};
-          acc = MFMA16(ldAx(xln, ST, mt * 16, 0, lane), b0, acc, 0, 0, 0);
-          acc = MFMA16(ldAx(xln, ST, mt * 16, 16, lane), b1, acc, 0, 0, 0);
-          acc = MFMA16(ldAx(xln, ST, mt * 16, 32, lane), b2, acc, 0, 0, 0);
-          acc = MFMA16(ldAx(xln, ST, mt * 16, 48, lane), b3, acc, 0, 0, 0);
-          int rb = mt * 16 + ((lane >> 4) << 2);
-#pragma unroll
-          for (int g = 0; g < 4; ++g)
-            P16[(rb + g) * (ST * 2) + col16] = f2bf_rn(fmaxf(acc[g], 0.f));
-        }
-      }
-      __syncthreads();
-      {
-        int roff = (nta * 16 + (lane & 15)) * 512 + chunk * 128;
-        int koff = (lane >> 4) << 3;
-        bf16x8 b0 = ldB<WSB>(f2Wb, f2W, roff + koff);
-        bf16x8 b1 = ldB<WSB>(f2Wb, f2W, roff + 32 + koff);
-        bf16x8 b2 = ldB<WSB>(f2Wb, f2W, roff + 64 + koff);
-        bf16x8 b3 = ldB<WSB>(f2Wb, f2W, roff + 96 + koff);
-#pragma unroll
-        for (int i = 0; i < 6; ++i) {
-          int mt = mha * 6 + i;
-          f32x4 a = acca[i];
-          a = MFMA16(ldAx(area, ST, mt * 16, 0, lane), b0, a, 0, 0, 0);
-          a = MFMA16(ldAx(area, ST, mt * 16, 16, lane), b1, a, 0, 0, 0);
-          a = MFMA16(ldAx(area, ST, mt * 16, 32, lane), b2, a, 0, 0, 0);
-          a = MFMA16(ldAx(area, ST, mt * 16, 48, lane), b3, a, 0, 0, 0);
-          acca[i] = a;
-        }
-      }
-      if (hasb) {
-        int roff = (ntb * 16 + (lane & 15)) * 512 + chunk * 128;
-        int koff = (lane >> 4) << 3;
-        bf16x8 b0 = ldB<WSB>(f2Wb, f2W, roff + koff);
-        bf16x8 b1 = ldB<WSB>(f2Wb, f2W, roff + 32 + koff);
-        bf16x8 b2 = ldB<WSB>(f2Wb, f2W, roff + 64 + koff);
-        bf16x8 b3 = ldB<WSB>(f2Wb, f2W, roff + 96 + koff);
-#pragma unroll
-        for (int i = 0; i < 6; ++i) {
-          int mt = mhb * 6 + i;
-          f32x4 a = accb[i];
-          a = MFMA16(ldAx(area, ST, mt * 16, 0, lane), b0, a, 0, 0, 0);
-          a = MFMA16(ldAx(area, ST, mt * 16, 16, lane), b1, a, 0, 0, 0);
-          a = MFMA16(ldAx(area, ST, mt * 16, 32, lane), b2, a, 0, 0, 0);
-          a = MFMA16(ldAx(area, ST, mt * 16, 48, lane), b3, a, 0, 0, 0);
-          accb[i] = a;
-        }
-      }
-      __syncthreads();
-    }
-    {
-      int col16 = nta * 16 + (lane & 15);
-#pragma unroll
-      for (int i = 0; i < 6; ++i) {
-        int rb = (mha * 6 + i) * 16 + ((lane >> 4) << 2);
-        f32x4 a = acca[i];
-#pragma unroll
-        for (int g = 0; g < 4; ++g) {
-          int a16 = (rb + g) * (ST * 2) + col16;
-          float old = __uint_as_float((unsigned)tok16[a16] << 16);
-          tok16[a16] = f2bf_rn(old + a[g]);
-        }
-      }
-    }
-    if (hasb) {
-      int col16 = ntb * 16 + (lane & 15);
-#pragma unroll
-      for (int i = 0; i < 6; ++i) {
-        int rb = (mhb * 6 + i) * 16 + ((lane >> 4) << 2);
-        f32x4 a = accb[i];
-#pragma unroll
-        for (int g = 0; g < 4; ++g) {
-          int a16 = (rb + g) * (ST * 2) + col16;
-          float old = __uint_as_float((unsigned)tok16[a16] << 16);
-          tok16[a16] = f2bf_rn(old + a[g]);
-        }
-      }
-    }
-  }
-  __syncthreads();
-
-  if (lrow < S_) {
-    float s = 0.f;
-#pragma unroll
-    for (int i = 0; i < 16; ++i) {
-      unsigned w = tokp[lrow * ST + lsub * 16 + i];
-      s += lo2f(w) + hi2f(w);
-    }
-    s += __shfl_xor(s, 1); s += __shfl_xor(s, 2);
-    float m = s * (1.f / 128.f);
-    float v = 0.f;
-#pragma unroll
-    for (int i = 0; i < 16; ++i) {
-      unsigned w = tokp[lrow * ST + lsub * 16 + i];
-      float t0 = lo2f(w) - m, t1 = hi2f(w) - m;
-      v = fmaf(t0, t0, v); v = fmaf(t1, t1, v);
-    }
-    v += __shfl_xor(v, 1); v += __shfl_xor(v, 2);
-    float rs = rsqrtf(v * (1.f / 128.f) + 1e-5f);
-#pragma unroll
-    for (int i = 0; i < 16; ++i) {
-      int d2 = lsub * 16 + i, d = 2 * d2;
-      unsigned w = tokp[lrow * ST + d2];
-      tokp[lrow * ST + d2] = pack2((lo2f(w) - m) * rs * p.plng[d] + p.plnb[d],
-                                   (hi2f(w) - m) * rs * p.plng[d + 1] + p.plnb[d + 1]);
+      for (int nt = 0; nt < 8; ++nt)
+        xln16[(row0 + g) * (XST * 2) + nt * 16 + colb] =
+            f2bf_rn((X[g][nt] - m) * rs * ga[nt] + be[nt]);
     }
   }
   __syncthreads();
@@ -660,11 +620,11 @@
     float s0 = 0.f, s1 = 0.f;
     int r = 0;
     for (; r + 2 <= S_; r += 2) {
-      unsigned w0 = tokp[r * ST + d2], w1 = tokp[(r + 1) * ST + d2];
+      unsigned w0 = xln[r * XST + d2], w1 = xln[(r + 1) * XST + d2];
       s0 += hi ? hi2f(w0) : lo2f(w0);
       s1 += hi ? hi2f(w1) : lo2f(w1);
     }
-    unsigned wl = tokp[(S_ - 1) * ST + d2];
+    unsigned wl = xln[(S_ - 1) * XST + d2];
     s0 += hi ? hi2f(wl) : lo2f(wl);
     areaF[PO_OFF + tid] = (s0 + s1) * (1.f / (float)S_);
   }
@@ -692,7 +652,7 @@
       float xr[16];
 #pragma unroll
       for (int i2 = 0; i2 < 8; ++i2) {
-        unsigned w = tokp[tid * ST + kb * 8 + i2];
+        unsigned w = xln[tid * XST + kb * 8 + i2];
         xr[2 * i2] = lo2f(w); xr[2 * i2 + 1] = hi2f(w);
       }
       const float *w = p.hxW1 + kb * 16;
@@ -743,7 +703,7 @@
         float xr[16];
 #pragma unroll
         for (int i2 = 0; i2 < 8; ++i2) {
-          unsigned w = tokp[r * ST + kb * 8 + i2];
+          unsigned w = xln[r * XST + kb * 8 + i2];
           xr[2 * i2] = lo2f(w); xr[2 * i2 + 1] = hi2f(w);
         }
         const float *w = p.tgW1 + kb * 16;
```

Result: slower. 3.489 ms (+67.4%).
